# Optimization experiments

Measured on AMD Instinct MI355X. Metric: run time of the kernel, lower is better.

Reference implementation:

```python
import jax, jax.numpy as jnp
import numpy as np

OPTION_NUM = 5
HEADS = 4
NUM_LAYERS = 3
N_NODES = 20000
N_EDGES = 640000
NODES_PER_GRAPH = 800
N_GRAPHS = 25          # N_NODES // NODES_PER_GRAPH, multiple of OPTION_NUM
N_GROUPS = 5           # N_GRAPHS // OPTION_NUM; must equal OPTION_NUM for output_layer
T_TOK = 256
TOKEN_DIM = 1024
D = 256                # out_channels
VOCAB = 100000


def setup_inputs() -> dict:
    key = jax.random.key(0)
    ks = jax.random.split(key, 16)
    nrm = lambda k, s: jax.random.normal(k, s, dtype=jnp.float32) * 0.05
    L = NUM_LAYERS
    return {
        "concept_ids": jax.random.randint(ks[0], (N_NODES,), 0, VOCAB, dtype=jnp.int32),
        "edge_index": jax.random.randint(ks[1], (2, N_EDGES), 0, N_NODES, dtype=jnp.int32),
        "edge_type": jax.random.randint(ks[2], (N_EDGES,), 0, 38, dtype=jnp.int32),
        "sentence_embeddings": nrm(ks[3], (N_GROUPS, TOKEN_DIM)),
        "token_embedding": nrm(ks[4], (N_GROUPS, T_TOK, TOKEN_DIM)),
        "batch": (jnp.arange(N_NODES, dtype=jnp.int32) // NODES_PER_GRAPH),
        "entity_embeddings": nrm(ks[5], (VOCAB, D)),
        "Wq": nrm(ks[6], (L, D, D)), "bq": jnp.zeros((L, D), jnp.float32),
        "Wk": nrm(ks[7], (L, D, D)), "bk": jnp.zeros((L, D), jnp.float32),
        "Wv": nrm(ks[8], (L, D, D)), "bv": jnp.zeros((L, D), jnp.float32),
        "Ws": nrm(ks[9], (L, TOKEN_DIM, D)), "bs": jnp.zeros((L, D), jnp.float32),
        "Wo": nrm(ks[10], (L, D, D)), "bo": jnp.zeros((L, D), jnp.float32),
        "W1": nrm(ks[11], (D, D)), "b1": jnp.zeros((D,), jnp.float32),
        "W2": nrm(ks[12], (TOKEN_DIM, D)), "b2": jnp.zeros((D,), jnp.float32),
        "W3": nrm(ks[13], (D, TOKEN_DIM)), "b3": jnp.zeros((TOKEN_DIM,), jnp.float32),
        "Wout": nrm(ks[14], (OPTION_NUM * D, D)), "bout": jnp.zeros((D,), jnp.float32),
    }


def reference(concept_ids, edge_index, edge_type, sentence_embeddings, token_embedding,
              batch, entity_embeddings, Wq, bq, Wk, bk, Wv, bv, Ws, bs, Wo, bo,
              W1, b1, W2, b2, W3, b3, Wout, bout):
    H = HEADS
    C = D // H
    sqdk = jnp.sqrt(jnp.float32(C))
    group = batch // OPTION_NUM                      # [N] in [0, N_GROUPS)
    row, col = edge_index[0], edge_index[1]

    x = entity_embeddings[concept_ids]               # [N, D]
    for l in range(NUM_LAYERS):
        Q = (x @ Wq[l] + bq[l]).reshape(-1, H, C)
        K = (x @ Wk[l] + bk[l]).reshape(-1, H, C)
        V = (x @ Wv[l] + bv[l]).reshape(-1, H, C)
        QS = (sentence_embeddings[group] @ Ws[l] + bs[l]).reshape(-1, H, C)
        Qi, Kj = Q[row], K[col]                      # [E, H, C]
        alpha = ((Qi * Kj).sum(-1) + (QS[row] * Kj).sum(-1) + (Qi * QS[col]).sum(-1)) / (3.0 * sqdk)
        alpha = jax.nn.leaky_relu(alpha, 0.2)
        alpha = jax.nn.softmax(alpha, axis=0)        # global softmax over edges (as in source)
        agg = jnp.zeros_like(V).at[row].add(V[col] * alpha[:, :, None])
        x = agg.reshape(-1, H * C) @ Wo[l] + bo[l] + x

    x = x @ W1 + b1                                  # [N, D]
    tok = token_embedding @ W2 + b2                  # [G, T, D]

    # attention_multihead (faithful double gather by group indices)
    scale = jnp.sqrt(jnp.float32(D))
    scores = jnp.einsum('nd,btd->bnt', x, tok) / scale   # [G, N, T]
    sel = scores[:, group, :]                            # gather dim 1
    w = jax.nn.softmax(sel, axis=-1)
    ao = jnp.einsum('bnt,btd->bnd', w, tok)              # [G, N, D]
    sel2 = ao[:, group, :]                               # second gather
    concat = jnp.transpose(sel2, (1, 0, 2)).reshape(x.shape[0], -1)  # [N, G*D]
    x = concat @ Wout + bout                             # [N, D]

    pooled = jax.ops.segment_max(x, batch, num_segments=N_GRAPHS)    # global_max_pool
    soft = pooled @ W3 + b3                              # [N_GRAPHS, token_dim]
    return soft.reshape(N_GRAPHS // OPTION_NUM, OPTION_NUM, -1)
```

## Files before the change

### kernel.cpp

```cpp
#include <hip/hip_runtime.h>
#include <hip/hip_bf16.h>

#define NNODES 20000
#define NEDGES 640000
#define DM 256
#define PAD 128

typedef short s16x8 __attribute__((ext_vector_type(8)));
typedef float f32x4 __attribute__((ext_vector_type(4)));
typedef float f32x2 __attribute__((ext_vector_type(2)));

__device__ inline float b2f(unsigned short u) {
  union { unsigned int i; float f; } z;
  z.i = (unsigned int)u << 16;
  return z.f;
}
__device__ inline unsigned short f2b(float f) {
  union { unsigned int i; float f; } z;
  z.f = f;
  unsigned int i = z.i;
  return (unsigned short)((i + 0x7FFFu + ((i >> 16) & 1u)) >> 16);
}

__device__ inline unsigned char f2fp8(float v) {
#if __has_builtin(__builtin_amdgcn_cvt_pk_fp8_f32)
  int t = __builtin_amdgcn_cvt_pk_fp8_f32(v, v, 0, false);
  return (unsigned char)(t & 0xFF);
#else
  union { float f; unsigned int u; } z;
  z.f = v;
  unsigned int s = (z.u >> 31) << 7;
  float av = fabsf(v);
  if (av >= 448.f) return (unsigned char)(s | 0x7E);
  if (av < 0.015625f) {
    int q = (int)rintf(av * 512.f);
    return (unsigned char)(s | (unsigned)q);
  }
  int e32 = (int)((z.u >> 23) & 255) - 127;
  unsigned mant = z.u & 0x7FFFFF;
  unsigned t = mant + 0x7FFFF + ((mant >> 20) & 1);
  if (t >= 0x800000u) { t = 0; e32++; }
  int e4 = e32 + 7;
  unsigned m3 = (t >> 20) & 7;
  if (e4 > 15 || (e4 == 15 && m3 == 7)) return (unsigned char)(s | 0x7E);
  return (unsigned char)(s | (unsigned)((e4 << 3) | m3));
#endif
}

__device__ inline float4 fp8x4_dec(unsigned int u) {
#if __has_builtin(__builtin_amdgcn_cvt_pk_f32_fp8)
  f32x2 lo = __builtin_amdgcn_cvt_pk_f32_fp8((int)u, false);
  f32x2 hi = __builtin_amdgcn_cvt_pk_f32_fp8((int)u, true);
  float4 r;
  r.x = lo[0]; r.y = lo[1]; r.z = hi[0]; r.w = hi[1];
  return r;
#else
  float4 r;
  float* p = &r.x;
#pragma unroll
  for (int j = 0; j < 4; j++) {
    unsigned b = (u >> (8 * j)) & 0xFF;
    unsigned s = b >> 7, e = (b >> 3) & 15, m = b & 7;
    float mag;
    if (e == 0) mag = (float)m * 0.001953125f;
    else {
      union { unsigned int i; float f; } z;
      z.i = ((e + 120u) << 23) | (m << 20);
      mag = z.f;
    }
    p[j] = s ? -mag : mag;
  }
  return r;
#endif
}

__global__ __launch_bounds__(256) void gather_kernel(
    const int* __restrict__ cid, const float* __restrict__ ent,
    float* __restrict__ x, unsigned short* __restrict__ xb,
    int* __restrict__ deg, float* __restrict__ sums, int n) {
  int idx = blockIdx.x * 256 + threadIdx.x;
  if (idx < NNODES) deg[idx] = 0;
  if (idx < 12) sums[idx] = 0.f;
  if (idx >= n * 64) return;
  int node = idx >> 6, d4 = idx & 63;
  float4 v = reinterpret_cast<const float4*>(ent)[(size_t)cid[node] * 64 + d4];
  reinterpret_cast<float4*>(x)[(size_t)node * 64 + d4] = v;
  ushort4 b;
  b.x = f2b(v.x); b.y = f2b(v.y); b.z = f2b(v.z); b.w = f2b(v.w);
  reinterpret_cast<ushort4*>(xb)[(size_t)node * 64 + d4] = b;
}

__global__ __launch_bounds__(256) void prep_kernel(
    const float* __restrict__ Wq, const float* __restrict__ Wk,
    const float* __restrict__ Wv, const float* __restrict__ Wo,
    unsigned short* __restrict__ WT, const float* __restrict__ W2,
    unsigned short* __restrict__ W2T, const float* __restrict__ te,
    unsigned short* __restrict__ tb, const float* __restrict__ sent,
    const float* __restrict__ Ws, const float* __restrict__ bs,
    float* __restrict__ QS5all) {
  int blk = blockIdx.x;
  if (blk < 3072) {
    int slot = blk >> 8;
    int l = slot >> 2, t = slot & 3;
    int n = blk & 255;
    int k = threadIdx.x;
    const float* src = (t == 0) ? Wq : (t == 1) ? Wk : (t == 2) ? Wv : Wo;
    WT[(size_t)slot * 65536 + n * 256 + k] =
        f2b(src[(size_t)l * 65536 + k * 256 + n]);
  } else if (blk < 4096) {
    int i = (blk - 3072) * 256 + threadIdx.x;
    int n = i >> 10, k = i & 1023;
    W2T[n * 1024 + k] = f2b(W2[k * 256 + n]);
  } else if (blk < 5376) {
    int i = (blk - 4096) * 256 + threadIdx.x;
    float4 v = reinterpret_cast<const float4*>(te)[i];
    ushort4 b;
    b.x = f2b(v.x); b.y = f2b(v.y); b.z = f2b(v.z); b.w = f2b(v.w);
    reinterpret_cast<ushort4*>(tb)[i] = b;
  } else {
    int idx = blk - 5376;
    int g = idx % 5, l = idx / 5;
    int j = threadIdx.x;
    __shared__ float sh[1024];
    for (int i = j; i < 1024; i += 256) sh[i] = sent[g * 1024 + i];
    __syncthreads();
    const float* W = Ws + (size_t)l * 1024 * 256;
    float acc = bs[l * 256 + j];
    for (int k = 0; k < 1024; k++) acc += sh[k] * W[k * 256 + j];
    QS5all[(size_t)(l * 5 + g) * 256 + j] = acc;
  }
}

__global__ __launch_bounds__(256) void fill_kernel(const int* __restrict__ ei,
                                                   const int* __restrict__ batch,
                                                   int* __restrict__ deg,
                                                   int* __restrict__ colPad,
                                                   int E) {
  int e = blockIdx.x * 256 + threadIdx.x;
  if (e >= E) return;
  int r = ei[e];
  int c = ei[E + e];
  int slot = atomicAdd(&deg[r], 1);
  if (slot < PAD) colPad[(size_t)r * PAD + slot] = c | ((batch[c] / 5) << 24);
}

__global__ __launch_bounds__(256) void qkv_gemm_kernel(
    const unsigned short* __restrict__ A, const unsigned short* __restrict__ Bt,
    const float* __restrict__ bq, const float* __restrict__ bk,
    const float* __restrict__ bv, float* __restrict__ Qf,
    unsigned char* __restrict__ KV8, int M) {
  int wid = threadIdx.x >> 6;
  int lane = threadIdx.x & 63;
  int wr = wid >> 1, wc = wid & 1;
  int rowBase = blockIdx.y * 64 + wr * 32;
  int colBase = blockIdx.x * 128 + wc * 64;
  int r16 = lane & 15, kg = lane >> 4;
  f32x4 acc[2][4] = {};
  for (int k0 = 0; k0 < 256; k0 += 32) {
    s16x8 a[2], b[4];
#pragma unroll
    for (int mi = 0; mi < 2; mi++) {
      int r = rowBase + mi * 16 + r16;
      s16x8 z = {};
      a[mi] = (r < M) ? *reinterpret_cast<const s16x8*>(
                            &A[(size_t)r * 256 + k0 + kg * 8])
                      : z;
    }
#pragma unroll
    for (int ni = 0; ni < 4; ni++) {
      int c = colBase + ni * 16 + r16;
      b[ni] = *reinterpret_cast<const s16x8*>(&Bt[(size_t)c * 256 + k0 + kg * 8]);
    }
#pragma unroll
    for (int mi = 0; mi < 2; mi++)
#pragma unroll
      for (int ni = 0; ni < 4; ni++)
        acc[mi][ni] = __builtin_amdgcn_mfma_f32_16x16x32_bf16(
            a[mi], b[ni], acc[mi][ni], 0, 0, 0);
  }
  int region = (blockIdx.x * 128) >> 8;
  const float* bias = (region == 0) ? bq : (region == 1) ? bk : bv;
  unsigned char* dstBase = KV8 + ((region == 1) ? 0 : 256);
#pragma unroll
  for (int mi = 0; mi < 2; mi++)
#pragma unroll
    for (int ni = 0; ni < 4; ni++) {
      int cg = colBase + ni * 16 + (lane & 15);
      int cr = cg & 255;
      float bia = bias[cr];
#pragma unroll
      for (int reg = 0; reg < 4; reg++) {
        int r = rowBase + mi * 16 + (lane >> 4) * 4 + reg;
        if (r >= M) continue;
        float v = acc[mi][ni][reg] + bia;
        if (region == 0)
          Qf[(size_t)r * 256 + cr] = v;
        else
          dstBase[(size_t)r * 512 + cr] = f2fp8(v);
      }
    }
}

__global__ __launch_bounds__(256) void gemm_bf16_kernel(
    const unsigned short* __restrict__ A, const unsigned short* __restrict__ Bt,
    const float* __restrict__ bias, const float* __restrict__ resid,
    float* __restrict__ Cf, unsigned short* __restrict__ Cb, int M, int K) {
  int wid = threadIdx.x >> 6;
  int lane = threadIdx.x & 63;
  int wr = wid >> 1, wc = wid & 1;
  int rowBase = blockIdx.y * 64 + wr * 32;
  int colBase = blockIdx.x * 128 + wc * 64;
  int r16 = lane & 15, kg = lane >> 4;
  f32x4 acc[2][4] = {};
  for (int k0 = 0; k0 < K; k0 += 32) {
    s16x8 a[2], b[4];
#pragma unroll
    for (int mi = 0; mi < 2; mi++) {
      int r = rowBase + mi * 16 + r16;
      s16x8 z = {};
      a[mi] = (r < M) ? *reinterpret_cast<const s16x8*>(
                            &A[(size_t)r * K + k0 + kg * 8])
                      : z;
    }
#pragma unroll
    for (int ni = 0; ni < 4; ni++) {
      int c = colBase + ni * 16 + r16;
      b[ni] = *reinterpret_cast<const s16x8*>(&Bt[(size_t)c * K + k0 + kg * 8]);
    }
#pragma unroll
    for (int mi = 0; mi < 2; mi++)
#pragma unroll
      for (int ni = 0; ni < 4; ni++)
        acc[mi][ni] = __builtin_amdgcn_mfma_f32_16x16x32_bf16(
            a[mi], b[ni], acc[mi][ni], 0, 0, 0);
  }
#pragma unroll
  for (int mi = 0; mi < 2; mi++)
#pragma unroll
    for (int ni = 0; ni < 4; ni++) {
      int c = colBase + ni * 16 + (lane & 15);
      float bia = bias[c];
#pragma unroll
      for (int reg = 0; reg < 4; reg++) {
        int r = rowBase + mi * 16 + (lane >> 4) * 4 + reg;
        if (r >= M) continue;
        float v = acc[mi][ni][reg] + bia;
        if (resid) v += resid[(size_t)r * 256 + c];
        if (Cf) Cf[(size_t)r * 256 + c] = v;
        if (Cb) Cb[(size_t)r * 256 + c] = f2b(v);
      }
    }
}

__global__ __launch_bounds__(256) void rescale_wo_kernel(
    unsigned short* __restrict__ WoT, const float* __restrict__ sums) {
  int i = blockIdx.x * 256 + threadIdx.x;
  int head = (i & 255) >> 6;
  WoT[i] = f2b(b2f(WoT[i]) / sums[head]);
}

template <int DO_AGG>
__global__ __launch_bounds__(256) void fused_edge_kernel(
    const int* __restrict__ deg, const int* __restrict__ colPad,
    const int* __restrict__ batch, const float* __restrict__ Q,
    const unsigned int* __restrict__ KV, const float* __restrict__ QS5,
    float* __restrict__ sums, unsigned short* __restrict__ aggb, int n) {
  int wv = __builtin_amdgcn_readfirstlane(threadIdx.x >> 6);
  int node = blockIdx.x * 4 + wv;
  int lane = threadIdx.x & 63;
  int head = lane >> 4;
  float sum0 = 0.f, sum1 = 0.f, sum2 = 0.f, sum3 = 0.f;
  float4 a0 = {0.f, 0.f, 0.f, 0.f}, a1 = a0, a2 = a0, a3 = a0;
  float4 qe = a0;
  float dq0 = 0.f, dq1 = 0.f, dq2 = 0.f, dq3 = 0.f, dq4 = 0.f;
  int dcount = 0;
  if (node < n) {
    float4 q = reinterpret_cast<const float4*>(Q)[(size_t)node * 64 + lane];
    int gr = batch[node] / 5;
    float4 qs = reinterpret_cast<const float4*>(QS5)[gr * 64 + lane];
    qe.x = q.x + qs.x; qe.y = q.y + qs.y; qe.z = q.z + qs.z; qe.w = q.w + qs.w;
#pragma unroll
    for (int g = 0; g < 5; g++) {
      float4 w = reinterpret_cast<const float4*>(QS5)[g * 64 + lane];
      float d = q.x * w.x + q.y * w.y + q.z * w.z + q.w * w.w;
      d += __shfl_xor(d, 1);
      d += __shfl_xor(d, 2);
      d += __shfl_xor(d, 4);
      d += __shfl_xor(d, 8);
      if (g == 0) dq0 = d;
      else if (g == 1) dq1 = d;
      else if (g == 2) dq2 = d;
      else if (g == 3) dq3 = d;
      else dq4 = d;
    }
    dcount = deg[node];
    if (dcount > PAD) dcount = PAD;
  }
  const int* myCol = colPad + (size_t)node * PAD;
  bool lead = (lane & 15) == 0;

  int ccc0 = 0, ccc1 = 0, ccc2 = 0, ccc3 = 0;
  unsigned krc0 = 0, krc1 = 0, krc2 = 0, krc3 = 0;
  unsigned vrc0 = 0, vrc1 = 0, vrc2 = 0, vrc3 = 0;
  if (dcount >= 4) {
    ccc0 = myCol[0]; ccc1 = myCol[1]; ccc2 = myCol[2]; ccc3 = myCol[3];
    krc0 = KV[(size_t)(ccc0 & 0xFFFFFF) * 128 + lane];
    krc1 = KV[(size_t)(ccc1 & 0xFFFFFF) * 128 + lane];
    krc2 = KV[(size_t)(ccc2 & 0xFFFFFF) * 128 + lane];
    krc3 = KV[(size_t)(ccc3 & 0xFFFFFF) * 128 + lane];
    if (DO_AGG) {
      vrc0 = KV[(size_t)(ccc0 & 0xFFFFFF) * 128 + 64 + lane];
      vrc1 = KV[(size_t)(ccc1 & 0xFFFFFF) * 128 + 64 + lane];
      vrc2 = KV[(size_t)(ccc2 & 0xFFFFFF) * 128 + 64 + lane];
      vrc3 = KV[(size_t)(ccc3 & 0xFFFFFF) * 128 + 64 + lane];
    }
  }
  int m = 0;
  for (; m + 4 <= dcount; m += 4) {
    int mn = m + 4;
    bool hn = (mn + 4 <= dcount);
    int ccn0 = 0, ccn1 = 0, ccn2 = 0, ccn3 = 0;
    unsigned krn0 = 0, krn1 = 0, krn2 = 0, krn3 = 0;
    unsigned vrn0 = 0, vrn1 = 0, vrn2 = 0, vrn3 = 0;
    if (hn) {
      ccn0 = myCol[mn]; ccn1 = myCol[mn + 1];
      ccn2 = myCol[mn + 2]; ccn3 = myCol[mn + 3];
      krn0 = KV[(size_t)(ccn0 & 0xFFFFFF) * 128 + lane];
      krn1 = KV[(size_t)(ccn1 & 0xFFFFFF) * 128 + lane];
      krn2 = KV[(size_t)(ccn2 & 0xFFFFFF) * 128 + lane];
      krn3 = KV[(size_t)(ccn3 & 0xFFFFFF) * 128 + lane];
      if (DO_AGG) {
        vrn0 = KV[(size_t)(ccn0 & 0xFFFFFF) * 128 + 64 + lane];
        vrn1 = KV[(size_t)(ccn1 & 0xFFFFFF) * 128 + 64 + lane];
        vrn2 = KV[(size_t)(ccn2 & 0xFFFFFF) * 128 + 64 + lane];
        vrn3 = KV[(size_t)(ccn3 & 0xFFFFFF) * 128 + 64 + lane];
      }
    }
    float4 kd0 = fp8x4_dec(krc0), kd1 = fp8x4_dec(krc1);
    float4 kd2 = fp8x4_dec(krc2), kd3 = fp8x4_dec(krc3);
    float p0 = qe.x * kd0.x + qe.y * kd0.y + qe.z * kd0.z + qe.w * kd0.w;
    float p1 = qe.x * kd1.x + qe.y * kd1.y + qe.z * kd1.z + qe.w * kd1.w;
    float p2 = qe.x * kd2.x + qe.y * kd2.y + qe.z * kd2.z + qe.w * kd2.w;
    float p3 = qe.x * kd3.x + qe.y * kd3.y + qe.z * kd3.z + qe.w * kd3.w;
    p0 += __shfl_xor(p0, 1); p1 += __shfl_xor(p1, 1);
    p2 += __shfl_xor(p2, 1); p3 += __shfl_xor(p3, 1);
    p0 += __shfl_xor(p0, 2); p1 += __shfl_xor(p1, 2);
    p2 += __shfl_xor(p2, 2); p3 += __shfl_xor(p3, 2);
    p0 += __shfl_xor(p0, 4); p1 += __shfl_xor(p1, 4);
    p2 += __shfl_xor(p2, 4); p3 += __shfl_xor(p3, 4);
    p0 += __shfl_xor(p0, 8); p1 += __shfl_xor(p1, 8);
    p2 += __shfl_xor(p2, 8); p3 += __shfl_xor(p3, 8);
    int gc0 = ccc0 >> 24, gc1 = ccc1 >> 24, gc2 = ccc2 >> 24, gc3 = ccc3 >> 24;
    float dv0 = (gc0 == 0) ? dq0 : (gc0 == 1) ? dq1 : (gc0 == 2) ? dq2 : (gc0 == 3) ? dq3 : dq4;
    float dv1 = (gc1 == 0) ? dq0 : (gc1 == 1) ? dq1 : (gc1 == 2) ? dq2 : (gc1 == 3) ? dq3 : dq4;
    float dv2 = (gc2 == 0) ? dq0 : (gc2 == 1) ? dq1 : (gc2 == 2) ? dq2 : (gc2 == 3) ? dq3 : dq4;
    float dv3 = (gc3 == 0) ? dq0 : (gc3 == 1) ? dq1 : (gc3 == 2) ? dq2 : (gc3 == 3) ? dq3 : dq4;
    float v0 = (p0 + dv0) * (1.f / 24.f); v0 = (v0 >= 0.f) ? v0 : 0.2f * v0;
    float v1 = (p1 + dv1) * (1.f / 24.f); v1 = (v1 >= 0.f) ? v1 : 0.2f * v1;
    float v2 = (p2 + dv2) * (1.f / 24.f); v2 = (v2 >= 0.f) ? v2 : 0.2f * v2;
    float v3 = (p3 + dv3) * (1.f / 24.f); v3 = (v3 >= 0.f) ? v3 : 0.2f * v3;
    float e0 = __expf(v0), e1 = __expf(v1), e2 = __expf(v2), e3 = __expf(v3);
    if (lead) { sum0 += e0; sum1 += e1; sum2 += e2; sum3 += e3; }
    if (DO_AGG) {
      float4 vd0 = fp8x4_dec(vrc0), vd1 = fp8x4_dec(vrc1);
      float4 vd2 = fp8x4_dec(vrc2), vd3 = fp8x4_dec(vrc3);
      a0.x += e0 * vd0.x; a0.y += e0 * vd0.y; a0.z += e0 * vd0.z; a0.w += e0 * vd0.w;
      a1.x += e1 * vd1.x; a1.y += e1 * vd1.y; a1.z += e1 * vd1.z; a1.w += e1 * vd1.w;
      a2.x += e2 * vd2.x; a2.y += e2 * vd2.y; a2.z += e2 * vd2.z; a2.w += e2 * vd2.w;
      a3.x += e3 * vd3.x; a3.y += e3 * vd3.y; a3.z += e3 * vd3.z; a3.w += e3 * vd3.w;
    }
    if (hn) {
      ccc0 = ccn0; ccc1 = ccn1; ccc2 = ccn2; ccc3 = ccn3;
      krc0 = krn0; krc1 = krn1; krc2 = krn2; krc3 = krn3;
      if (DO_AGG) { vrc0 = vrn0; vrc1 = vrn1; vrc2 = vrn2; vrc3 = vrn3; }
    }
  }
  for (; m < dcount; m++) {
    int cc = myCol[m];
    int c = cc & 0xFFFFFF, gc = cc >> 24;
    float4 kd = fp8x4_dec(KV[(size_t)c * 128 + lane]);
    float p = qe.x * kd.x + qe.y * kd.y + qe.z * kd.z + qe.w * kd.w;
    p += __shfl_xor(p, 1);
    p += __shfl_xor(p, 2);
    p += __shfl_xor(p, 4);
    p += __shfl_xor(p, 8);
    float dqv = (gc == 0) ? dq0 : (gc == 1) ? dq1 : (gc == 2) ? dq2
                : (gc == 3) ? dq3 : dq4;
    float v = (p + dqv) * (1.f / 24.f);
    v = (v >= 0.f) ? v : 0.2f * v;
    float ev = __expf(v);
    if (lead) sum0 += ev;
    if (DO_AGG) {
      float4 vd = fp8x4_dec(KV[(size_t)c * 128 + 64 + lane]);
      a0.x += ev * vd.x; a0.y += ev * vd.y; a0.z += ev * vd.z; a0.w += ev * vd.w;
    }
  }
  float sumExp = (sum0 + sum1) + (sum2 + sum3);
  if (DO_AGG && node < n) {
    float4 acc;
    acc.x = (a0.x + a1.x) + (a2.x + a3.x);
    acc.y = (a0.y + a1.y) + (a2.y + a3.y);
    acc.z = (a0.z + a1.z) + (a2.z + a3.z);
    acc.w = (a0.w + a1.w) + (a2.w + a3.w);
    ushort4 b;
    b.x = f2b(acc.x); b.y = f2b(acc.y); b.z = f2b(acc.z); b.w = f2b(acc.w);
    reinterpret_cast<ushort4*>(aggb)[(size_t)node * 64 + lane] = b;
  }
  __shared__ float red[4][4];
  int w = threadIdx.x >> 6;
  if (lead) red[w][head] = sumExp;
  __syncthreads();
  if (threadIdx.x < 4) {
    float t = red[0][threadIdx.x] + red[1][threadIdx.x] + red[2][threadIdx.x] +
              red[3][threadIdx.x];
    atomicAdd(&sums[threadIdx.x], t);
  }
}

__global__ __launch_bounds__(1024) void tail_head_kernel(
    const int* __restrict__ deg, const int* __restrict__ colPad,
    const int* __restrict__ batch, const float* __restrict__ Q,
    const unsigned int* __restrict__ KV, const float* __restrict__ QS5,
    const float* __restrict__ sums, const float* __restrict__ Wo2,
    const float* __restrict__ bo2, const float* __restrict__ x,
    const float* __restrict__ W1, const float* __restrict__ b1,
    float* __restrict__ x1) {
  __shared__ float a0s[256];
  __shared__ float t1[256];
  __shared__ float part[4][256];
  int tid = threadIdx.x;
  if (tid < 64) {
    int lane = tid;
    int head = lane >> 4;
    float4 q = reinterpret_cast<const float4*>(Q)[lane];
    int gr = batch[0] / 5;
    float4 qs = reinterpret_cast<const float4*>(QS5)[gr * 64 + lane];
    float4 qe = {q.x + qs.x, q.y + qs.y, q.z + qs.z, q.w + qs.w};
    float dq0 = 0.f, dq1 = 0.f, dq2 = 0.f, dq3 = 0.f, dq4 = 0.f;
#pragma unroll
    for (int g = 0; g < 5; g++) {
      float4 w = reinterpret_cast<const float4*>(QS5)[g * 64 + lane];
      float d = q.x * w.x + q.y * w.y + q.z * w.z + q.w * w.w;
      d += __shfl_xor(d, 1);
      d += __shfl_xor(d, 2);
      d += __shfl_xor(d, 4);
      d += __shfl_xor(d, 8);
      if (g == 0) dq0 = d;
      else if (g == 1) dq1 = d;
      else if (g == 2) dq2 = d;
      else if (g == 3) dq3 = d;
      else dq4 = d;
    }
    float4 acc = {0.f, 0.f, 0.f, 0.f};
    int dcount = deg[0];
    if (dcount > PAD) dcount = PAD;
    for (int m = 0; m < dcount; m++) {
      int cc = colPad[m];
      int c = cc & 0xFFFFFF, gc = cc >> 24;
      float4 kd = fp8x4_dec(KV[(size_t)c * 128 + lane]);
      float p = qe.x * kd.x + qe.y * kd.y + qe.z * kd.z + qe.w * kd.w;
      p += __shfl_xor(p, 1);
      p += __shfl_xor(p, 2);
      p += __shfl_xor(p, 4);
      p += __shfl_xor(p, 8);
      float dqv = (gc == 0) ? dq0 : (gc == 1) ? dq1 : (gc == 2) ? dq2
                  : (gc == 3) ? dq3 : dq4;
      float v = (p + dqv) * (1.f / 24.f);
      v = (v >= 0.f) ? v : 0.2f * v;
      float ev = __expf(v);
      float4 vd = fp8x4_dec(KV[(size_t)c * 128 + 64 + lane]);
      acc.x += ev * vd.x;
      acc.y += ev * vd.y;
      acc.z += ev * vd.z;
      acc.w += ev * vd.w;
    }
    float invS = 1.f / sums[head];
    a0s[lane * 4 + 0] = acc.x * invS;
    a0s[lane * 4 + 1] = acc.y * invS;
    a0s[lane * 4 + 2] = acc.z * invS;
    a0s[lane * 4 + 3] = acc.w * invS;
  }
  __syncthreads();
  int j = tid & 255, s = tid >> 8;
  float acc = 0.f;
#pragma unroll 8
  for (int k = s * 64; k < s * 64 + 64; k++) acc += a0s[k] * Wo2[k * 256 + j];
  part[s][j] = acc;
  __syncthreads();
  if (tid < 256)
    t1[tid] = part[0][tid] + part[1][tid] + part[2][tid] + part[3][tid] +
              bo2[tid] + x[tid];
  __syncthreads();
  float acc2 = 0.f;
#pragma unroll 8
  for (int k = s * 64; k < s * 64 + 64; k++) acc2 += t1[k] * W1[k * 256 + j];
  part[s][j] = acc2;
  __syncthreads();
  if (tid < 256)
    x1[tid] = part[0][tid] + part[1][tid] + part[2][tid] + part[3][tid] +
              b1[tid];
}

__global__ __launch_bounds__(256) void attn_out_kernel(
    const float* __restrict__ x1g, const float* __restrict__ tok,
    float* __restrict__ AO) {
  int b = blockIdx.x;
  int tid = threadIdx.x;
  int wave = tid >> 6, lane = tid & 63;
  int sub = lane >> 4, l16 = lane & 15;
  __shared__ float x1s[256];
  __shared__ float scs[256];
  __shared__ float red[256];
  __shared__ float wgt[256];
  x1s[tid] = x1g[tid];
  __syncthreads();
  const float4* xv4 = reinterpret_cast<const float4*>(x1s);
  for (int it = 0; it < 16; it++) {
    int row = wave * 64 + it * 4 + sub;
    const float4* tr =
        reinterpret_cast<const float4*>(tok + (size_t)(b * 256 + row) * 256);
    float sc = 0.f;
#pragma unroll
    for (int q = 0; q < 4; q++) {
      float4 v = tr[l16 + q * 16];
      float4 xv = xv4[l16 + q * 16];
      sc += v.x * xv.x + v.y * xv.y + v.z * xv.z + v.w * xv.w;
    }
    sc += __shfl_xor(sc, 1);
    sc += __shfl_xor(sc, 2);
    sc += __shfl_xor(sc, 4);
    sc += __shfl_xor(sc, 8);
    if (l16 == 0) scs[row] = sc * (1.f / 16.f);
  }
  __syncthreads();
  float sc = scs[tid];
  red[tid] = sc;
  __syncthreads();
  for (int off = 128; off; off >>= 1) {
    if (tid < off) red[tid] = fmaxf(red[tid], red[tid + off]);
    __syncthreads();
  }
  float mx = red[0];
  __syncthreads();
  float ex = expf(sc - mx);
  red[tid] = ex;
  __syncthreads();
  for (int off = 128; off; off >>= 1) {
    if (tid < off) red[tid] += red[tid + off];
    __syncthreads();
  }
  wgt[tid] = ex / red[0];
  __syncthreads();
  float acc = 0.f;
#pragma unroll 4
  for (int k = 0; k < 256; k++)
    acc += wgt[k] * tok[(size_t)(b * 256 + k) * 256 + tid];
  AO[b * 256 + tid] = acc;
}

__global__ __launch_bounds__(256) void final_y_kernel(
    const float* __restrict__ AO, const float* __restrict__ Wout,
    float* __restrict__ partial) {
  int s = blockIdx.x;
  int j = threadIdx.x;
  __shared__ float a[80];
  if (threadIdx.x < 80) a[threadIdx.x] = AO[s * 80 + threadIdx.x];
  __syncthreads();
  const float* W = Wout + (size_t)s * 80 * 256;
  float acc = 0.f;
#pragma unroll 8
  for (int k = 0; k < 80; k++) acc += a[k] * W[k * 256 + j];
  partial[s * 256 + j] = acc;
}

__global__ __launch_bounds__(256) void final_out2_kernel(
    const float* __restrict__ partial, const float* __restrict__ bout,
    const float* __restrict__ W3, const float* __restrict__ b3,
    float* __restrict__ out) {
  __shared__ float y[256];
  int j = threadIdx.x;
  float acc = bout[j];
#pragma unroll
  for (int s = 0; s < 16; s++) acc += partial[s * 256 + j];
  y[j] = acc;
  __syncthreads();
  int t = blockIdx.x * 256 + j;
  float o = b3[t];
#pragma unroll 8
  for (int k = 0; k < 256; k++) o += y[k] * W3[k * 1024 + t];
  for (int g = 0; g < 25; g++) out[(size_t)g * 1024 + t] = o;
}

extern "C" void kernel_launch(void* const* d_in, const int* in_sizes, int n_in,
                              void* d_out, int out_size, void* d_ws,
                              size_t ws_size, hipStream_t stream) {
  const int* concept_ids = (const int*)d_in[0];
  const int* edge_index = (const int*)d_in[1];
  const float* sent = (const float*)d_in[3];
  const float* tokemb = (const float*)d_in[4];
  const int* batch = (const int*)d_in[5];
  const float* ent = (const float*)d_in[6];
  const float* Wq = (const float*)d_in[7];
  const float* bq = (const float*)d_in[8];
  const float* Wk = (const float*)d_in[9];
  const float* bk = (const float*)d_in[10];
  const float* Wv = (const float*)d_in[11];
  const float* bv = (const float*)d_in[12];
  const float* Ws = (const float*)d_in[13];
  const float* bs = (const float*)d_in[14];
  const float* Wo = (const float*)d_in[15];
  const float* bo = (const float*)d_in[16];
  const float* W1 = (const float*)d_in[17];
  const float* b1 = (const float*)d_in[18];
  const float* W2 = (const float*)d_in[19];
  const float* b2 = (const float*)d_in[20];
  const float* W3 = (const float*)d_in[21];
  const float* b3 = (const float*)d_in[22];
  const float* Wout = (const float*)d_in[23];
  const float* bout = (const float*)d_in[24];
  float* out = (float*)d_out;

  float* ws = (float*)d_ws;
  size_t off_ = 0;
  auto alloc = [&](size_t n) {
    float* p = ws + off_;
    off_ += n;
    return p;
  };
  float* x = alloc((size_t)NNODES * DM);
  float* x2 = alloc((size_t)NNODES * DM);
  float* Qf = alloc((size_t)NNODES * DM);
  unsigned short* xb = (unsigned short*)alloc((size_t)NNODES * DM / 2);
  unsigned short* aggb = (unsigned short*)alloc((size_t)NNODES * DM / 2);
  unsigned char* KV8 = (unsigned char*)alloc((size_t)NNODES * DM / 2);
  unsigned short* WT = (unsigned short*)alloc(12 * 65536 / 2);
  unsigned short* W2T = (unsigned short*)alloc(262144 / 2);
  unsigned short* tokb = (unsigned short*)alloc(1280 * 1024 / 2);
  float* tok = alloc(1280 * 256);
  float* QS5all = alloc(3 * 5 * 256);
  float* sums = alloc(16);
  float* x1 = alloc(256);
  float* AO = alloc(1280);
  float* partial = alloc(16 * 256);
  int* deg = (int*)alloc(NNODES);
  int* colPad = (int*)alloc((size_t)NNODES * PAD);

  gather_kernel<<<5000, 256, 0, stream>>>(concept_ids, ent, x, xb, deg, sums,
                                          NNODES);
  prep_kernel<<<5391, 256, 0, stream>>>(Wq, Wk, Wv, Wo, WT, W2, W2T, tokemb,
                                        tokb, sent, Ws, bs, QS5all);
  fill_kernel<<<(NEDGES + 255) / 256, 256, 0, stream>>>(edge_index, batch, deg,
                                                        colPad, NEDGES);

  float* xin = x;
  float* xout = x2;
  for (int l = 0; l < 3; l++) {
    unsigned short* WoT = WT + (size_t)(l * 4 + 3) * 65536;
    {
      dim3 g(6, (NNODES + 63) / 64);
      qkv_gemm_kernel<<<g, 256, 0, stream>>>(
          xb, WT + (size_t)(l * 4) * 65536, bq + l * DM, bk + l * DM,
          bv + l * DM, Qf, KV8, NNODES);
    }
    if (l < 2) {
      fused_edge_kernel<1><<<5000, 256, 0, stream>>>(
          deg, colPad, batch, Qf, (const unsigned int*)KV8,
          QS5all + l * 1280, sums + l * 4, aggb, NNODES);
      rescale_wo_kernel<<<256, 256, 0, stream>>>(WoT, sums + l * 4);
      dim3 g(2, (NNODES + 63) / 64);
      gemm_bf16_kernel<<<g, 256, 0, stream>>>(aggb, WoT, bo + l * DM, xin,
                                              xout, xb, NNODES, 256);
      float* tmp = xin;
      xin = xout;
      xout = tmp;
    } else {
      fused_edge_kernel<0><<<5000, 256, 0, stream>>>(
          deg, colPad, batch, Qf, (const unsigned int*)KV8,
          QS5all + l * 1280, sums + l * 4, nullptr, NNODES);
      tail_head_kernel<<<1, 1024, 0, stream>>>(
          deg, colPad, batch, Qf, (const unsigned int*)KV8, QS5all + l * 1280,
          sums + l * 4, Wo + (size_t)2 * 65536, bo + 2 * DM, xin, W1, b1, x1);
    }
  }

  {
    dim3 g(2, 1280 / 64);
    gemm_bf16_kernel<<<g, 256, 0, stream>>>(tokb, W2T, b2, nullptr, tok,
                                            nullptr, 1280, 1024);
  }
  attn_out_kernel<<<5, 256, 0, stream>>>(x1, tok, AO);
  final_y_kernel<<<16, 256, 0, stream>>>(AO, Wout, partial);
  final_out2_kernel<<<4, 256, 0, stream>>>(partial, bout, W3, b3, out);
}
```

Measured before the change: 638.6 us.

## Store Q in bf16, widen GEMM tiles, skip V projection in last layer

Q is now written and read as bf16 rather than fp32, which halves Q traffic in the edge kernels. The QKV and output GEMMs use 128-column warp tiles, so each block covers the full 256 columns with fewer blocks and more accumulator registers per thread. The last layer skips computing V: the tail kernel aggregates bf16 x for node 0 per head and applies Wv and the bias afterwards. The software prefetch in the edge loop is removed in favour of direct loads. The larger tiles raise register pressure and may reduce occupancy, and dropping the prefetch may expose gather latency.

```diff
diff --git a/kernel.cpp b/kernel.cpp
--- a/kernel.cpp
+++ b/kernel.cpp
@@ -147,17 +147,18 @@
 __global__ __launch_bounds__(256) void qkv_gemm_kernel(
     const unsigned short* __restrict__ A, const unsigned short* __restrict__ Bt,
     const float* __restrict__ bq, const float* __restrict__ bk,
-    const float* __restrict__ bv, float* __restrict__ Qf,
+    const float* __restrict__ bv, unsigned short* __restrict__ Qb,
     unsigned char* __restrict__ KV8, int M) {
   int wid = threadIdx.x >> 6;
   int lane = threadIdx.x & 63;
   int wr = wid >> 1, wc = wid & 1;
   int rowBase = blockIdx.y * 64 + wr * 32;
-  int colBase = blockIdx.x * 128 + wc * 64;
+  int region = blockIdx.x;
+  int colBase = region * 256 + wc * 128;
   int r16 = lane & 15, kg = lane >> 4;
-  f32x4 acc[2][4] = {};
+  f32x4 acc[2][8] = {};
   for (int k0 = 0; k0 < 256; k0 += 32) {
-    s16x8 a[2], b[4];
+    s16x8 a[2], b[8];
 #pragma unroll
     for (int mi = 0; mi < 2; mi++) {
       int r = rowBase + mi * 16 + r16;
@@ -167,24 +168,23 @@
                       : z;
     }
 #pragma unroll
-    for (int ni = 0; ni < 4; ni++) {
+    for (int ni = 0; ni < 8; ni++) {
       int c = colBase + ni * 16 + r16;
       b[ni] = *reinterpret_cast<const s16x8*>(&Bt[(size_t)c * 256 + k0 + kg * 8]);
     }
 #pragma unroll
     for (int mi = 0; mi < 2; mi++)
 #pragma unroll
-      for (int ni = 0; ni < 4; ni++)
+      for (int ni = 0; ni < 8; ni++)
         acc[mi][ni] = __builtin_amdgcn_mfma_f32_16x16x32_bf16(
             a[mi], b[ni], acc[mi][ni], 0, 0, 0);
   }
-  int region = (blockIdx.x * 128) >> 8;
   const float* bias = (region == 0) ? bq : (region == 1) ? bk : bv;
   unsigned char* dstBase = KV8 + ((region == 1) ? 0 : 256);
 #pragma unroll
   for (int mi = 0; mi < 2; mi++)
 #pragma unroll
-    for (int ni = 0; ni < 4; ni++) {
+    for (int ni = 0; ni < 8; ni++) {
       int cg = colBase + ni * 16 + (lane & 15);
       int cr = cg & 255;
       float bia = bias[cr];
@@ -194,7 +194,7 @@
         if (r >= M) continue;
         float v = acc[mi][ni][reg] + bia;
         if (region == 0)
-          Qf[(size_t)r * 256 + cr] = v;
+          Qb[(size_t)r * 256 + cr] = f2b(v);
         else
           dstBase[(size_t)r * 512 + cr] = f2fp8(v);
       }
@@ -209,11 +209,11 @@
   int lane = threadIdx.x & 63;
   int wr = wid >> 1, wc = wid & 1;
   int rowBase = blockIdx.y * 64 + wr * 32;
-  int colBase = blockIdx.x * 128 + wc * 64;
+  int colBase = wc * 128;
   int r16 = lane & 15, kg = lane >> 4;
-  f32x4 acc[2][4] = {};
+  f32x4 acc[2][8] = {};
   for (int k0 = 0; k0 < K; k0 += 32) {
-    s16x8 a[2], b[4];
+    s16x8 a[2], b[8];
 #pragma unroll
     for (int mi = 0; mi < 2; mi++) {
       int r = rowBase + mi * 16 + r16;
@@ -223,21 +223,21 @@
                       : z;
     }
 #pragma unroll
-    for (int ni = 0; ni < 4; ni++) {
+    for (int ni = 0; ni < 8; ni++) {
       int c = colBase + ni * 16 + r16;
       b[ni] = *reinterpret_cast<const s16x8*>(&Bt[(size_t)c * K + k0 + kg * 8]);
     }
 #pragma unroll
     for (int mi = 0; mi < 2; mi++)
 #pragma unroll
-      for (int ni = 0; ni < 4; ni++)
+      for (int ni = 0; ni < 8; ni++)
         acc[mi][ni] = __builtin_amdgcn_mfma_f32_16x16x32_bf16(
             a[mi], b[ni], acc[mi][ni], 0, 0, 0);
   }
 #pragma unroll
   for (int mi = 0; mi < 2; mi++)
 #pragma unroll
-    for (int ni = 0; ni < 4; ni++) {
+    for (int ni = 0; ni < 8; ni++) {
       int c = colBase + ni * 16 + (lane & 15);
       float bia = bias[c];
 #pragma unroll
@@ -262,7 +262,7 @@
 template <int DO_AGG>
 __global__ __launch_bounds__(256) void fused_edge_kernel(
     const int* __restrict__ deg, const int* __restrict__ colPad,
-    const int* __restrict__ batch, const float* __restrict__ Q,
+    const int* __restrict__ batch, const unsigned short* __restrict__ Qb,
     const unsigned int* __restrict__ KV, const float* __restrict__ QS5,
     float* __restrict__ sums, unsigned short* __restrict__ aggb, int n) {
   int wv = __builtin_amdgcn_readfirstlane(threadIdx.x >> 6);
@@ -275,7 +275,9 @@
   float dq0 = 0.f, dq1 = 0.f, dq2 = 0.f, dq3 = 0.f, dq4 = 0.f;
   int dcount = 0;
   if (node < n) {
-    float4 q = reinterpret_cast<const float4*>(Q)[(size_t)node * 64 + lane];
+    ushort4 qu =
+        reinterpret_cast<const ushort4*>(Qb)[(size_t)node * 64 + lane];
+    float4 q = {b2f(qu.x), b2f(qu.y), b2f(qu.z), b2f(qu.w)};
     int gr = batch[node] / 5;
     float4 qs = reinterpret_cast<const float4*>(QS5)[gr * 64 + lane];
     qe.x = q.x + qs.x; qe.y = q.y + qs.y; qe.z = q.z + qs.z; qe.w = q.w + qs.w;
@@ -298,46 +300,25 @@
   }
   const int* myCol = colPad + (size_t)node * PAD;
   bool lead = (lane & 15) == 0;
-
-  int ccc0 = 0, ccc1 = 0, ccc2 = 0, ccc3 = 0;
-  unsigned krc0 = 0, krc1 = 0, krc2 = 0, krc3 = 0;
-  unsigned vrc0 = 0, vrc1 = 0, vrc2 = 0, vrc3 = 0;
-  if (dcount >= 4) {
-    ccc0 = myCol[0]; ccc1 = myCol[1]; ccc2 = myCol[2]; ccc3 = myCol[3];
-    krc0 = KV[(size_t)(ccc0 & 0xFFFFFF) * 128 + lane];
-    krc1 = KV[(size_t)(ccc1 & 0xFFFFFF) * 128 + lane];
-    krc2 = KV[(size_t)(ccc2 & 0xFFFFFF) * 128 + lane];
-    krc3 = KV[(size_t)(ccc3 & 0xFFFFFF) * 128 + lane];
-    if (DO_AGG) {
-      vrc0 = KV[(size_t)(ccc0 & 0xFFFFFF) * 128 + 64 + lane];
-      vrc1 = KV[(size_t)(ccc1 & 0xFFFFFF) * 128 + 64 + lane];
-      vrc2 = KV[(size_t)(ccc2 & 0xFFFFFF) * 128 + 64 + lane];
-      vrc3 = KV[(size_t)(ccc3 & 0xFFFFFF) * 128 + 64 + lane];
-    }
-  }
   int m = 0;
   for (; m + 4 <= dcount; m += 4) {
-    int mn = m + 4;
-    bool hn = (mn + 4 <= dcount);
-    int ccn0 = 0, ccn1 = 0, ccn2 = 0, ccn3 = 0;
-    unsigned krn0 = 0, krn1 = 0, krn2 = 0, krn3 = 0;
-    unsigned vrn0 = 0, vrn1 = 0, vrn2 = 0, vrn3 = 0;
-    if (hn) {
-      ccn0 = myCol[mn]; ccn1 = myCol[mn + 1];
-      ccn2 = myCol[mn + 2]; ccn3 = myCol[mn + 3];
-      krn0 = KV[(size_t)(ccn0 & 0xFFFFFF) * 128 + lane];
-      krn1 = KV[(size_t)(ccn1 & 0xFFFFFF) * 128 + lane];
-      krn2 = KV[(size_t)(ccn2 & 0xFFFFFF) * 128 + lane];
-      krn3 = KV[(size_t)(ccn3 & 0xFFFFFF) * 128 + lane];
-      if (DO_AGG) {
-        vrn0 = KV[(size_t)(ccn0 & 0xFFFFFF) * 128 + 64 + lane];
-        vrn1 = KV[(size_t)(ccn1 & 0xFFFFFF) * 128 + 64 + lane];
-        vrn2 = KV[(size_t)(ccn2 & 0xFFFFFF) * 128 + 64 + lane];
-        vrn3 = KV[(size_t)(ccn3 & 0xFFFFFF) * 128 + 64 + lane];
-      }
-    }
-    float4 kd0 = fp8x4_dec(krc0), kd1 = fp8x4_dec(krc1);
-    float4 kd2 = fp8x4_dec(krc2), kd3 = fp8x4_dec(krc3);
+    int cc0 = myCol[m + 0], cc1 = myCol[m + 1];
+    int cc2 = myCol[m + 2], cc3 = myCol[m + 3];
+    int c0 = cc0 & 0xFFFFFF, c1 = cc1 & 0xFFFFFF;
+    int c2 = cc2 & 0xFFFFFF, c3 = cc3 & 0xFFFFFF;
+    unsigned int kr0 = KV[(size_t)c0 * 128 + lane];
+    unsigned int kr1 = KV[(size_t)c1 * 128 + lane];
+    unsigned int kr2 = KV[(size_t)c2 * 128 + lane];
+    unsigned int kr3 = KV[(size_t)c3 * 128 + lane];
+    unsigned int vr0 = 0, vr1 = 0, vr2 = 0, vr3 = 0;
+    if (DO_AGG) {
+      vr0 = KV[(size_t)c0 * 128 + 64 + lane];
+      vr1 = KV[(size_t)c1 * 128 + 64 + lane];
+      vr2 = KV[(size_t)c2 * 128 + 64 + lane];
+      vr3 = KV[(size_t)c3 * 128 + 64 + lane];
+    }
+    float4 kd0 = fp8x4_dec(kr0), kd1 = fp8x4_dec(kr1);
+    float4 kd2 = fp8x4_dec(kr2), kd3 = fp8x4_dec(kr3);
     float p0 = qe.x * kd0.x + qe.y * kd0.y + qe.z * kd0.z + qe.w * kd0.w;
     float p1 = qe.x * kd1.x + qe.y * kd1.y + qe.z * kd1.z + qe.w * kd1.w;
     float p2 = qe.x * kd2.x + qe.y * kd2.y + qe.z * kd2.z + qe.w * kd2.w;
@@ -350,7 +331,7 @@
     p2 += __shfl_xor(p2, 4); p3 += __shfl_xor(p3, 4);
     p0 += __shfl_xor(p0, 8); p1 += __shfl_xor(p1, 8);
     p2 += __shfl_xor(p2, 8); p3 += __shfl_xor(p3, 8);
-    int gc0 = ccc0 >> 24, gc1 = ccc1 >> 24, gc2 = ccc2 >> 24, gc3 = ccc3 >> 24;
+    int gc0 = cc0 >> 24, gc1 = cc1 >> 24, gc2 = cc2 >> 24, gc3 = cc3 >> 24;
     float dv0 = (gc0 == 0) ? dq0 : (gc0 == 1) ? dq1 : (gc0 == 2) ? dq2 : (gc0 == 3) ? dq3 : dq4;
     float dv1 = (gc1 == 0) ? dq0 : (gc1 == 1) ? dq1 : (gc1 == 2) ? dq2 : (gc1 == 3) ? dq3 : dq4;
     float dv2 = (gc2 == 0) ? dq0 : (gc2 == 1) ? dq1 : (gc2 == 2) ? dq2 : (gc2 == 3) ? dq3 : dq4;
@@ -362,17 +343,12 @@
     float e0 = __expf(v0), e1 = __expf(v1), e2 = __expf(v2), e3 = __expf(v3);
     if (lead) { sum0 += e0; sum1 += e1; sum2 += e2; sum3 += e3; }
     if (DO_AGG) {
-      float4 vd0 = fp8x4_dec(vrc0), vd1 = fp8x4_dec(vrc1);
-      float4 vd2 = fp8x4_dec(vrc2), vd3 = fp8x4_dec(vrc3);
+      float4 vd0 = fp8x4_dec(vr0), vd1 = fp8x4_dec(vr1);
+      float4 vd2 = fp8x4_dec(vr2), vd3 = fp8x4_dec(vr3);
       a0.x += e0 * vd0.x; a0.y += e0 * vd0.y; a0.z += e0 * vd0.z; a0.w += e0 * vd0.w;
       a1.x += e1 * vd1.x; a1.y += e1 * vd1.y; a1.z += e1 * vd1.z; a1.w += e1 * vd1.w;
       a2.x += e2 * vd2.x; a2.y += e2 * vd2.y; a2.z += e2 * vd2.z; a2.w += e2 * vd2.w;
       a3.x += e3 * vd3.x; a3.y += e3 * vd3.y; a3.z += e3 * vd3.z; a3.w += e3 * vd3.w;
-    }
-    if (hn) {
-      ccc0 = ccn0; ccc1 = ccn1; ccc2 = ccn2; ccc3 = ccn3;
-      krc0 = krn0; krc1 = krn1; krc2 = krn2; krc3 = krn3;
-      if (DO_AGG) { vrc0 = vrn0; vrc1 = vrn1; vrc2 = vrn2; vrc3 = vrn3; }
     }
   }
   for (; m < dcount; m++) {
@@ -419,12 +395,15 @@
 
 __global__ __launch_bounds__(1024) void tail_head_kernel(
     const int* __restrict__ deg, const int* __restrict__ colPad,
-    const int* __restrict__ batch, const float* __restrict__ Q,
-    const unsigned int* __restrict__ KV, const float* __restrict__ QS5,
-    const float* __restrict__ sums, const float* __restrict__ Wo2,
-    const float* __restrict__ bo2, const float* __restrict__ x,
-    const float* __restrict__ W1, const float* __restrict__ b1,
-    float* __restrict__ x1) {
+    const int* __restrict__ batch, const unsigned short* __restrict__ Qb,
+    const unsigned int* __restrict__ KV, const unsigned short* __restrict__ xb,
+    const float* __restrict__ QS5, const float* __restrict__ sums,
+    const float* __restrict__ Wv2, const float* __restrict__ bv2,
+    const float* __restrict__ Wo2, const float* __restrict__ bo2,
+    const float* __restrict__ x, const float* __restrict__ W1,
+    const float* __restrict__ b1, float* __restrict__ x1) {
+  __shared__ float xh[4][256];
+  __shared__ float sE4[4];
   __shared__ float a0s[256];
   __shared__ float t1[256];
   __shared__ float part[4][256];
@@ -432,7 +411,8 @@
   if (tid < 64) {
     int lane = tid;
     int head = lane >> 4;
-    float4 q = reinterpret_cast<const float4*>(Q)[lane];
+    ushort4 qu = reinterpret_cast<const ushort4*>(Qb)[lane];
+    float4 q = {b2f(qu.x), b2f(qu.y), b2f(qu.z), b2f(qu.w)};
     int gr = batch[0] / 5;
     float4 qs = reinterpret_cast<const float4*>(QS5)[gr * 64 + lane];
     float4 qe = {q.x + qs.x, q.y + qs.y, q.z + qs.z, q.w + qs.w};
@@ -451,7 +431,8 @@
       else if (g == 3) dq3 = d;
       else dq4 = d;
     }
-    float4 acc = {0.f, 0.f, 0.f, 0.f};
+    float4 xaccA = {0, 0, 0, 0}, xaccB = xaccA, xaccC = xaccA, xaccD = xaccA;
+    float sE = 0.f;
     int dcount = deg[0];
     if (dcount > PAD) dcount = PAD;
     for (int m = 0; m < dcount; m++) {
@@ -468,20 +449,42 @@
       float v = (p + dqv) * (1.f / 24.f);
       v = (v >= 0.f) ? v : 0.2f * v;
       float ev = __expf(v);
-      float4 vd = fp8x4_dec(KV[(size_t)c * 128 + 64 + lane]);
-      acc.x += ev * vd.x;
-      acc.y += ev * vd.y;
-      acc.z += ev * vd.z;
-      acc.w += ev * vd.w;
-    }
-    float invS = 1.f / sums[head];
-    a0s[lane * 4 + 0] = acc.x * invS;
-    a0s[lane * 4 + 1] = acc.y * invS;
-    a0s[lane * 4 + 2] = acc.z * invS;
-    a0s[lane * 4 + 3] = acc.w * invS;
+      sE += ev;
+      float e0 = __shfl(ev, 0);
+      float e1 = __shfl(ev, 16);
+      float e2 = __shfl(ev, 32);
+      float e3 = __shfl(ev, 48);
+      ushort4 xu = reinterpret_cast<const ushort4*>(xb)[(size_t)c * 64 + lane];
+      float4 xv = {b2f(xu.x), b2f(xu.y), b2f(xu.z), b2f(xu.w)};
+      xaccA.x += e0 * xv.x; xaccA.y += e0 * xv.y; xaccA.z += e0 * xv.z; xaccA.w += e0 * xv.w;
+      xaccB.x += e1 * xv.x; xaccB.y += e1 * xv.y; xaccB.z += e1 * xv.z; xaccB.w += e1 * xv.w;
+      xaccC.x += e2 * xv.x; xaccC.y += e2 * xv.y; xaccC.z += e2 * xv.z; xaccC.w += e2 * xv.w;
+      xaccD.x += e3 * xv.x; xaccD.y += e3 * xv.y; xaccD.z += e3 * xv.z; xaccD.w += e3 * xv.w;
+    }
+    xh[0][lane * 4 + 0] = xaccA.x; xh[0][lane * 4 + 1] = xaccA.y;
+    xh[0][lane * 4 + 2] = xaccA.z; xh[0][lane * 4 + 3] = xaccA.w;
+    xh[1][lane * 4 + 0] = xaccB.x; xh[1][lane * 4 + 1] = xaccB.y;
+    xh[1][lane * 4 + 2] = xaccB.z; xh[1][lane * 4 + 3] = xaccB.w;
+    xh[2][lane * 4 + 0] = xaccC.x; xh[2][lane * 4 + 1] = xaccC.y;
+    xh[2][lane * 4 + 2] = xaccC.z; xh[2][lane * 4 + 3] = xaccC.w;
+    xh[3][lane * 4 + 0] = xaccD.x; xh[3][lane * 4 + 1] = xaccD.y;
+    xh[3][lane * 4 + 2] = xaccD.z; xh[3][lane * 4 + 3] = xaccD.w;
+    if ((lane & 15) == 0) sE4[head] = sE;
   }
   __syncthreads();
   int j = tid & 255, s = tid >> 8;
+  int hj = j >> 6;
+  float accv = 0.f;
+#pragma unroll 8
+  for (int k = s * 64; k < s * 64 + 64; k++) accv += xh[hj][k] * Wv2[k * 256 + j];
+  part[s][j] = accv;
+  __syncthreads();
+  if (tid < 256) {
+    float tot = part[0][tid] + part[1][tid] + part[2][tid] + part[3][tid] +
+                sE4[hj] * bv2[tid];
+    a0s[tid] = tot / sums[hj];
+  }
+  __syncthreads();
   float acc = 0.f;
 #pragma unroll 8
   for (int k = s * 64; k < s * 64 + 64; k++) acc += a0s[k] * Wo2[k * 256 + j];
@@ -629,7 +632,7 @@
   };
   float* x = alloc((size_t)NNODES * DM);
   float* x2 = alloc((size_t)NNODES * DM);
-  float* Qf = alloc((size_t)NNODES * DM);
+  unsigned short* Qb = (unsigned short*)alloc((size_t)NNODES * DM / 2);
   unsigned short* xb = (unsigned short*)alloc((size_t)NNODES * DM / 2);
   unsigned short* aggb = (unsigned short*)alloc((size_t)NNODES * DM / 2);
   unsigned char* KV8 = (unsigned char*)alloc((size_t)NNODES * DM / 2);
@@ -657,17 +660,17 @@
   for (int l = 0; l < 3; l++) {
     unsigned short* WoT = WT + (size_t)(l * 4 + 3) * 65536;
     {
-      dim3 g(6, (NNODES + 63) / 64);
+      dim3 g((l < 2) ? 3 : 2, (NNODES + 63) / 64);
       qkv_gemm_kernel<<<g, 256, 0, stream>>>(
           xb, WT + (size_t)(l * 4) * 65536, bq + l * DM, bk + l * DM,
-          bv + l * DM, Qf, KV8, NNODES);
+          bv + l * DM, Qb, KV8, NNODES);
     }
     if (l < 2) {
       fused_edge_kernel<1><<<5000, 256, 0, stream>>>(
-          deg, colPad, batch, Qf, (const unsigned int*)KV8,
-          QS5all + l * 1280, sums + l * 4, aggb, NNODES);
+          deg, colPad, batch, Qb, (const unsigned int*)KV8, QS5all + l * 1280,
+          sums + l * 4, aggb, NNODES);
       rescale_wo_kernel<<<256, 256, 0, stream>>>(WoT, sums + l * 4);
-      dim3 g(2, (NNODES + 63) / 64);
+      dim3 g(1, (NNODES + 63) / 64);
       gemm_bf16_kernel<<<g, 256, 0, stream>>>(aggb, WoT, bo + l * DM, xin,
                                               xout, xb, NNODES, 256);
       float* tmp = xin;
@@ -675,16 +678,17 @@
       xout = tmp;
     } else {
       fused_edge_kernel<0><<<5000, 256, 0, stream>>>(
-          deg, colPad, batch, Qf, (const unsigned int*)KV8,
-          QS5all + l * 1280, sums + l * 4, nullptr, NNODES);
+          deg, colPad, batch, Qb, (const unsigned int*)KV8, QS5all + l * 1280,
+          sums + l * 4, nullptr, NNODES);
       tail_head_kernel<<<1, 1024, 0, stream>>>(
-          deg, colPad, batch, Qf, (const unsigned int*)KV8, QS5all + l * 1280,
-          sums + l * 4, Wo + (size_t)2 * 65536, bo + 2 * DM, xin, W1, b1, x1);
+          deg, colPad, batch, Qb, (const unsigned int*)KV8, xb,
+          QS5all + l * 1280, sums + l * 4, Wv + (size_t)2 * 65536,
+          bv + 2 * DM, Wo + (size_t)2 * 65536, bo + 2 * DM, xin, W1, b1, x1);
     }
   }
 
   {
-    dim3 g(2, 1280 / 64);
+    dim3 g(1, 1280 / 64);
     gemm_bf16_kernel<<<g, 256, 0, stream>>>(tokb, W2T, b2, nullptr, tok,
                                             nullptr, 1280, 1024);
   }
```

Result: slower. 691.2 us (+8.3%).
